# Optimization experiments

Measured on AMD Instinct MI355X. Metric: run time of the kernel, lower is better.

Reference implementation:

```python
import jax, jax.numpy as jnp
import numpy as np

N, K, IN_C, OUT_C = 100000, 128, 128, 128


def setup_inputs() -> dict:
    key = jax.random.key(0)
    k1, k2, k3 = jax.random.split(key, 3)
    x = jax.random.normal(k1, (N, IN_C), dtype=jnp.float32)
    U = jax.random.normal(k2, (N, K), dtype=jnp.float32)
    coeffs = jax.random.normal(k3, (OUT_C, K, IN_C), dtype=jnp.float32)
    return {"x": x, "U": U, "coeffs": coeffs}


def reference(x, U, coeffs):
    # U.T @ x : (K, in_channels)
    spec = jnp.einsum('nk,ni->ki', U, x)
    # coeffs * spec, summed over in_channels : (out_channels, K)
    mixed = jnp.einsum('oki,ki->ok', coeffs, spec)
    # U @ mixed : (out_channels, N)
    out = jnp.einsum('nk,ok->on', U, mixed)
    # softmax over N (dim=-1), then transpose -> (N, out_channels)
    return jax.nn.softmax(out, axis=-1).T
```

## Files before the change

kernel.cpp:

```cpp
#include <hip/hip_runtime.h>
#include <math.h>

#define N_PTS 100000
#define KDIM 128
#define CDIM 128
#define TILE_N 64
#define NB1 ((N_PTS + TILE_N - 1) / TILE_N)

typedef short s16x8 __attribute__((ext_vector_type(8)));
typedef float f32x4 __attribute__((ext_vector_type(4)));

static __device__ __forceinline__ unsigned short f2bf(float f) {
    unsigned int u = __float_as_uint(f);
    unsigned int r = (u + 0x7FFFu + ((u >> 16) & 1u)) >> 16;
    return (unsigned short)r;
}
static __device__ __forceinline__ float bf2f(unsigned short h) {
    return __uint_as_float(((unsigned int)h) << 16);
}

static __device__ __forceinline__ void split_trunc(float v, unsigned short& hi, unsigned short& lo) {
    unsigned int u = __float_as_uint(v);
    unsigned int uh = u & 0xFFFF0000u;
    float lf = v - __uint_as_float(uh);
    hi = (unsigned short)(u >> 16);
    lo = (unsigned short)(__float_as_uint(lf) >> 16);
}

static __device__ __forceinline__ void block_sync_lds() {
    asm volatile("s_waitcnt lgkmcnt(0)" ::: "memory");
    __builtin_amdgcn_s_barrier();
    asm volatile("" ::: "memory");
}

__global__ __launch_bounds__(512, 4) void kA(const float* __restrict__ U,
                                             const float* __restrict__ x,
                                             float* __restrict__ partials,
                                             int chunk) {
    __shared__ unsigned short SB[2][4][4096];
    const int tid = threadIdx.x;
    const int b = blockIdx.x;
    const int n_begin = b * chunk;
    const int n_end = min(N_PTS, n_begin + chunk);
    const int lane = tid & 63;
    const int w = tid >> 6;
    const int mtb = (w & 3) * 2;
    const int ntb = (w >> 2) * 4;
    const int quad = lane >> 4;
    const int nl = lane & 15;

    const int sc = tid & 127;
    const int rq = tid >> 7;
    const int sgran = (sc >> 4) * 64 + rq * 16 + (sc & 15);

    f32x4 acc[2][4];
#pragma unroll
    for (int mi = 0; mi < 2; ++mi)
#pragma unroll
        for (int ni = 0; ni < 4; ++ni) acc[mi][ni] = (f32x4)(0.0f);

    float uvA[8], xvA[8], uvB[8], xvB[8];

    auto loadChunk = [&](int ci, float* uv, float* xv) {
        const int r0 = n_begin + ci * 32 + rq * 8;
#pragma unroll
        for (int jj = 0; jj < 8; ++jj) {
            int gn = r0 + jj;
            bool ok = (gn < n_end);
            uv[jj] = ok ? U[(size_t)gn * 128 + sc] : 0.0f;
            xv[jj] = ok ? x[(size_t)gn * 128 + sc] : 0.0f;
        }
    };

    auto splitWrite = [&](int buf, const float* uv, const float* xv) {
        s16x8 uh, ul, xh, xl;
#pragma unroll
        for (int jj = 0; jj < 8; ++jj) {
            unsigned short h, l;
            split_trunc(uv[jj], h, l);
            uh[jj] = (short)h; ul[jj] = (short)l;
            split_trunc(xv[jj], h, l);
            xh[jj] = (short)h; xl[jj] = (short)l;
        }
        *(s16x8*)&SB[buf][0][sgran * 8] = uh;
        *(s16x8*)&SB[buf][1][sgran * 8] = ul;
        *(s16x8*)&SB[buf][2][sgran * 8] = xh;
        *(s16x8*)&SB[buf][3][sgran * 8] = xl;
    };

    auto compute = [&](int buf) {
        s16x8 ah[2], al[2];
#pragma unroll
        for (int mi = 0; mi < 2; ++mi) {
            const int off = ((mtb + mi) * 64 + lane) * 8;
            ah[mi] = *(s16x8*)&SB[buf][0][off];
            al[mi] = *(s16x8*)&SB[buf][1][off];
        }
#pragma unroll
        for (int ni = 0; ni < 4; ++ni) {
            const int off = ((ntb + ni) * 64 + lane) * 8;
            s16x8 bh = *(s16x8*)&SB[buf][2][off];
            s16x8 bl = *(s16x8*)&SB[buf][3][off];
#pragma unroll
            for (int mi = 0; mi < 2; ++mi) {
                acc[mi][ni] = __builtin_amdgcn_mfma_f32_16x16x32_bf16(ah[mi], bh, acc[mi][ni], 0, 0, 0);
                acc[mi][ni] = __builtin_amdgcn_mfma_f32_16x16x32_bf16(al[mi], bh, acc[mi][ni], 0, 0, 0);
                acc[mi][ni] = __builtin_amdgcn_mfma_f32_16x16x32_bf16(ah[mi], bl, acc[mi][ni], 0, 0, 0);
            }
        }
    };

    loadChunk(0, uvA, xvA);
    splitWrite(0, uvA, xvA);
    loadChunk(1, uvB, xvB);
    block_sync_lds();

    const int nTrips = chunk >> 6;
    for (int t = 0; t < nTrips; ++t) {
        loadChunk(2 * t + 2, uvA, xvA);
        compute(0);
        splitWrite(1, uvB, xvB);
        block_sync_lds();
        loadChunk(2 * t + 3, uvB, xvB);
        compute(1);
        if (t + 1 < nTrips) splitWrite(0, uvA, xvA);
        block_sync_lds();
    }

    float* p = partials + (size_t)b * 16384;
#pragma unroll
    for (int mi = 0; mi < 2; ++mi) {
#pragma unroll
        for (int reg = 0; reg < 4; ++reg) {
            int k = (mtb + mi) * 16 + quad * 4 + reg;
#pragma unroll
            for (int ni = 0; ni < 4; ++ni) {
                int i = (ntb + ni) * 16 + nl;
                p[k * 128 + i] = acc[mi][ni][reg];
            }
        }
    }
}

__global__ __launch_bounds__(256) void kA2a(const float* __restrict__ partials,
                                            float* __restrict__ partial2, int nA) {
    const int jc = blockIdx.x >> 3;
    const int s = blockIdx.x & 7;
    const int j = jc * 256 + threadIdx.x;
    const int per = (nA + 7) >> 3;
    int b = s * per;
    const int be = min(b + per, nA);
    float a0 = 0.0f, a1 = 0.0f, a2 = 0.0f, a3 = 0.0f;
    for (; b + 4 <= be; b += 4) {
        a0 += partials[(size_t)(b + 0) * 16384 + j];
        a1 += partials[(size_t)(b + 1) * 16384 + j];
        a2 += partials[(size_t)(b + 2) * 16384 + j];
        a3 += partials[(size_t)(b + 3) * 16384 + j];
    }
    for (; b < be; ++b) a0 += partials[(size_t)b * 16384 + j];
    partial2[(size_t)s * 16384 + j] = (a0 + a1) + (a2 + a3);
}

__global__ __launch_bounds__(256) void kB(const float* __restrict__ coeffs,
                                          const float* __restrict__ partial2,
                                          unsigned short* __restrict__ afrag_hi,
                                          unsigned short* __restrict__ afrag_lo) {
    int wave = (blockIdx.x * 256 + threadIdx.x) >> 6;
    int lane = threadIdx.x & 63;
    int o = wave >> 7;
    int k = wave & 127;
    const int j = k * 128 + lane * 2;
    float2 p0 = *(const float2*)&partial2[j];
    float2 p1 = *(const float2*)&partial2[16384 + j];
    float2 p2 = *(const float2*)&partial2[2 * 16384 + j];
    float2 p3 = *(const float2*)&partial2[3 * 16384 + j];
    float2 p4 = *(const float2*)&partial2[4 * 16384 + j];
    float2 p5 = *(const float2*)&partial2[5 * 16384 + j];
    float2 p6 = *(const float2*)&partial2[6 * 16384 + j];
    float2 p7 = *(const float2*)&partial2[7 * 16384 + j];
    float sx = ((p0.x + p1.x) + (p2.x + p3.x)) + ((p4.x + p5.x) + (p6.x + p7.x));
    float sy = ((p0.y + p1.y) + (p2.y + p3.y)) + ((p4.y + p5.y) + (p6.y + p7.y));
    float2 c2 = *(const float2*)&coeffs[((size_t)o * 128 + k) * 128 + lane * 2];
    float v = c2.x * sx + c2.y * sy;
#pragma unroll
    for (int s = 32; s >= 1; s >>= 1) v += __shfl_xor(v, s);
    if (lane == 0) {
        unsigned short hi = f2bf(v);
        unsigned short lo = f2bf(v - bf2f(hi));
        int idx = ((o >> 4) * 4 + (k >> 5)) * 512 + (((k >> 3) & 3) * 16 + (o & 15)) * 8 + (k & 7);
        afrag_hi[idx] = hi;
        afrag_lo[idx] = lo;
    }
}

__global__ __launch_bounds__(512) void kC1(const float* __restrict__ U,
                                           const unsigned short* __restrict__ afrag_hi,
                                           const unsigned short* __restrict__ afrag_lo,
                                           float* __restrict__ out,
                                           float* __restrict__ m_part,
                                           float* __restrict__ l_part) {
    __shared__ unsigned short Bh[8192];
    __shared__ unsigned short Bl[8192];
    const int tid = threadIdx.x;
    const int b = blockIdx.x;
    const int n0 = b * TILE_N;
    const int lane = tid & 63;
    const int w = tid >> 6;
    const int quad = lane >> 4;
    const int nl = lane & 15;

    {
        const int sn = tid & 63;
        const int k8b = tid >> 6;
        const int gn = n0 + sn;
#pragma unroll
        for (int r = 0; r < 2; ++r) {
            const int k0 = (k8b + r * 8) * 8;
            float4 f0 = make_float4(0, 0, 0, 0), f1 = make_float4(0, 0, 0, 0);
            if (gn < N_PTS) {
                f0 = *(const float4*)&U[(size_t)gn * 128 + k0];
                f1 = *(const float4*)&U[(size_t)gn * 128 + k0 + 4];
            }
            float vv[8] = {f0.x, f0.y, f0.z, f0.w, f1.x, f1.y, f1.z, f1.w};
            s16x8 hh, ll;
#pragma unroll
            for (int jj = 0; jj < 8; ++jj) {
                unsigned short h, l;
                split_trunc(vv[jj], h, l);
                hh[jj] = (short)h;
                ll[jj] = (short)l;
            }
            const int T = (k0 >> 5) * 4 + (sn >> 4);
            const int g = T * 64 + ((k0 >> 3) & 3) * 16 + ((sn & 15) ^ (T & 3));
            *(s16x8*)&Bh[g * 8] = hh;
            *(s16x8*)&Bl[g * 8] = ll;
        }
    }

    s16x8 Ah[4], Al[4];
#pragma unroll
    for (int kc = 0; kc < 4; ++kc) {
        size_t aoff = (size_t)(w * 4 + kc) * 512 + lane * 8;
        Ah[kc] = *(const s16x8*)(afrag_hi + aoff);
        Al[kc] = *(const s16x8*)(afrag_lo + aoff);
    }

    __syncthreads();

    f32x4 acc[4];
#pragma unroll
    for (int nt = 0; nt < 4; ++nt) acc[nt] = (f32x4)(0.0f);

#pragma unroll
    for (int kc = 0; kc < 4; ++kc) {
#pragma unroll
        for (int nt = 0; nt < 4; ++nt) {
            const int T = kc * 4 + nt;
            const int g = T * 64 + quad * 16 + (nl ^ (T & 3));
            s16x8 bh = *(s16x8*)&Bh[g * 8];
            s16x8 bl = *(s16x8*)&Bl[g * 8];
            acc[nt] = __builtin_amdgcn_mfma_f32_16x16x32_bf16(Ah[kc], bh, acc[nt], 0, 0, 0);
            acc[nt] = __builtin_amdgcn_mfma_f32_16x16x32_bf16(Al[kc], bh, acc[nt], 0, 0, 0);
            acc[nt] = __builtin_amdgcn_mfma_f32_16x16x32_bf16(Ah[kc], bl, acc[nt], 0, 0, 0);
        }
    }

#pragma unroll
    for (int nt = 0; nt < 4; ++nt) {
        if (n0 + nt * 16 + nl >= N_PTS) {
#pragma unroll
            for (int reg = 0; reg < 4; ++reg) acc[nt][reg] = -3.4e38f;
        }
    }

    float mb[4];
#pragma unroll
    for (int reg = 0; reg < 4; ++reg)
        mb[reg] = fmaxf(fmaxf(acc[0][reg], acc[1][reg]), fmaxf(acc[2][reg], acc[3][reg]));
#pragma unroll
    for (int s = 1; s < 16; s <<= 1) {
#pragma unroll
        for (int reg = 0; reg < 4; ++reg) mb[reg] = fmaxf(mb[reg], __shfl_xor(mb[reg], s));
    }

#pragma unroll
    for (int nt = 0; nt < 4; ++nt) {
#pragma unroll
        for (int reg = 0; reg < 4; ++reg) acc[nt][reg] = __expf(acc[nt][reg] - mb[reg]);
        int gn = n0 + nt * 16 + nl;
        if (gn < N_PTS)
            *(f32x4*)&out[(size_t)gn * 128 + w * 16 + quad * 4] = acc[nt];
    }

    float ls[4];
#pragma unroll
    for (int reg = 0; reg < 4; ++reg)
        ls[reg] = ((acc[0][reg] + acc[1][reg]) + (acc[2][reg] + acc[3][reg]));
#pragma unroll
    for (int s = 1; s < 16; s <<= 1) {
#pragma unroll
        for (int reg = 0; reg < 4; ++reg) ls[reg] += __shfl_xor(ls[reg], s);
    }

    if (nl == 0) {
#pragma unroll
        for (int reg = 0; reg < 4; ++reg) {
            int o = w * 16 + quad * 4 + reg;
            m_part[(size_t)o * NB1 + b] = mb[reg];
            l_part[(size_t)o * NB1 + b] = ls[reg];
        }
    }
}

__global__ __launch_bounds__(256) void kC2(const float* __restrict__ m_part,
                                           const float* __restrict__ l_part,
                                           float* __restrict__ scale) {
    const int o = blockIdx.x;
    const int tid = threadIdx.x;
    const float* __restrict__ mp = m_part + (size_t)o * NB1;
    const float* __restrict__ lp = l_part + (size_t)o * NB1;
    __shared__ float sm[256];
    float m = -3.4e38f;
    for (int b = tid; b < NB1; b += 256) m = fmaxf(m, mp[b]);
    sm[tid] = m;
    __syncthreads();
    for (int s = 128; s >= 1; s >>= 1) {
        if (tid < s) sm[tid] = fmaxf(sm[tid], sm[tid + s]);
        __syncthreads();
    }
    m = sm[0];
    __syncthreads();
    float l = 0.0f;
    for (int b = tid; b < NB1; b += 256)
        l += lp[b] * __expf(mp[b] - m);
    sm[tid] = l;
    __syncthreads();
    for (int s = 128; s >= 1; s >>= 1) {
        if (tid < s) sm[tid] += sm[tid + s];
        __syncthreads();
    }
    l = sm[0];
    float inv = 1.0f / l;
    for (int b = tid; b < NB1; b += 256)
        scale[(size_t)o * NB1 + b] = __expf(mp[b] - m) * inv;
}

__global__ __launch_bounds__(256) void kC3(float* __restrict__ out,
                                           const float* __restrict__ scale) {
    const int b = blockIdx.x;
    const int tid = threadIdx.x;
    __shared__ float sc[128];
    if (tid < 128) sc[tid] = scale[(size_t)tid * NB1 + b];
    __syncthreads();
    const int n0 = b * TILE_N;
#pragma unroll
    for (int r = 0; r < 8; ++r) {
        int idx = (r * 256 + tid) * 4;
        int n = idx >> 7;
        int o = idx & 127;
        int gn = n0 + n;
        if (gn < N_PTS) {
            float4 v = *(float4*)&out[(size_t)gn * 128 + o];
            v.x *= sc[o];
            v.y *= sc[o + 1];
            v.z *= sc[o + 2];
            v.w *= sc[o + 3];
            *(float4*)&out[(size_t)gn * 128 + o] = v;
        }
    }
}

extern "C" void kernel_launch(void* const* d_in, const int* in_sizes, int n_in,
                              void* d_out, int out_size, void* d_ws, size_t ws_size,
                              hipStream_t stream) {
    const float* x = (const float*)d_in[0];
    const float* U = (const float*)d_in[1];
    const float* coeffs = (const float*)d_in[2];
    float* out = (float*)d_out;

    float* f = (float*)d_ws;
    float* spec = f;
    unsigned short* afrag_hi = (unsigned short*)(f + 16384);
    unsigned short* afrag_lo = (unsigned short*)(f + 16384 + 8192);
    float* m_part = f + 16384 + 16384;
    float* l_part = m_part + (size_t)128 * NB1;
    float* scale = l_part + (size_t)128 * NB1;
    float* partial2 = scale + (size_t)128 * NB1;
    float* partialsA = partial2 + 8 * 16384;
    (void)spec;

    size_t fixed_bytes = ((size_t)(16384 * 2) + (size_t)NB1 * 128 * 3 + (size_t)8 * 16384) * 4;
    int nA = 1024;
    if (ws_size > fixed_bytes) {
        size_t avail = (ws_size - fixed_bytes) / 65536;
        if ((size_t)nA > avail) nA = (int)avail;
    } else {
        nA = 1;
    }
    if (nA < 1) nA = 1;
    int chunk = (((N_PTS + nA - 1) / nA) + 63) & ~63;
    int nB = (N_PTS + chunk - 1) / chunk;

    kA<<<nB, 512, 0, stream>>>(U, x, partialsA, chunk);
    kA2a<<<512, 256, 0, stream>>>(partialsA, partial2, nB);
    kB<<<4096, 256, 0, stream>>>(coeffs, partial2, afrag_hi, afrag_lo);
    kC1<<<NB1, 512, 0, stream>>>(U, afrag_hi, afrag_lo, out, m_part, l_part);
    kC2<<<128, 256, 0, stream>>>(m_part, l_part, scale);
    kC3<<<NB1, 256, 0, stream>>>(out, scale);
}
```

Measured before the change: 207.9 us.

## Recompute U@mixed tile in final pass instead of storing and rescaling output

The output stage now runs the small GEMM twice: a first pass that only produces per-tile max and exp-sum statistics, and a second pass that recomputes the tile and writes the fully normalized softmax directly. This removes the write-then-read-modify-write of the full 51 MB output that the separate scaling kernel needed, at the cost of reading U and doing the MFMA work twice. Separately, kA drops LDS double buffering in favour of a single buffer with an extra barrier per chunk and asks for 8 waves per SIMD occupancy, trading intra-block overlap for more resident blocks.

```diff
diff --git a/kernel.cpp b/kernel.cpp
--- a/kernel.cpp
+++ b/kernel.cpp
@@ -33,11 +33,11 @@
     asm volatile("" ::: "memory");
 }
 
-__global__ __launch_bounds__(512, 4) void kA(const float* __restrict__ U,
+__global__ __launch_bounds__(512, 8) void kA(const float* __restrict__ U,
                                              const float* __restrict__ x,
                                              float* __restrict__ partials,
                                              int chunk) {
-    __shared__ unsigned short SB[2][4][4096];
+    __shared__ unsigned short SB[4][4096];
     const int tid = threadIdx.x;
     const int b = blockIdx.x;
     const int n_begin = b * chunk;
@@ -72,7 +72,7 @@
         }
     };
 
-    auto splitWrite = [&](int buf, const float* uv, const float* xv) {
+    auto splitWrite = [&](const float* uv, const float* xv) {
         s16x8 uh, ul, xh, xl;
 #pragma unroll
         for (int jj = 0; jj < 8; ++jj) {
@@ -82,25 +82,25 @@
             split_trunc(xv[jj], h, l);
             xh[jj] = (short)h; xl[jj] = (short)l;
         }
-        *(s16x8*)&SB[buf][0][sgran * 8] = uh;
-        *(s16x8*)&SB[buf][1][sgran * 8] = ul;
-        *(s16x8*)&SB[buf][2][sgran * 8] = xh;
-        *(s16x8*)&SB[buf][3][sgran * 8] = xl;
+        *(s16x8*)&SB[0][sgran * 8] = uh;
+        *(s16x8*)&SB[1][sgran * 8] = ul;
+        *(s16x8*)&SB[2][sgran * 8] = xh;
+        *(s16x8*)&SB[3][sgran * 8] = xl;
     };
 
-    auto compute = [&](int buf) {
+    auto compute = [&]() {
         s16x8 ah[2], al[2];
 #pragma unroll
         for (int mi = 0; mi < 2; ++mi) {
             const int off = ((mtb + mi) * 64 + lane) * 8;
-            ah[mi] = *(s16x8*)&SB[buf][0][off];
-            al[mi] = *(s16x8*)&SB[buf][1][off];
+            ah[mi] = *(s16x8*)&SB[0][off];
+            al[mi] = *(s16x8*)&SB[1][off];
         }
 #pragma unroll
         for (int ni = 0; ni < 4; ++ni) {
             const int off = ((ntb + ni) * 64 + lane) * 8;
-            s16x8 bh = *(s16x8*)&SB[buf][2][off];
-            s16x8 bl = *(s16x8*)&SB[buf][3][off];
+            s16x8 bh = *(s16x8*)&SB[2][off];
+            s16x8 bl = *(s16x8*)&SB[3][off];
 #pragma unroll
             for (int mi = 0; mi < 2; ++mi) {
                 acc[mi][ni] = __builtin_amdgcn_mfma_f32_16x16x32_bf16(ah[mi], bh, acc[mi][ni], 0, 0, 0);
@@ -111,19 +111,18 @@
     };
 
     loadChunk(0, uvA, xvA);
-    splitWrite(0, uvA, xvA);
-    loadChunk(1, uvB, xvB);
-    block_sync_lds();
 
     const int nTrips = chunk >> 6;
     for (int t = 0; t < nTrips; ++t) {
+        loadChunk(2 * t + 1, uvB, xvB);
+        splitWrite(uvA, xvA);
+        block_sync_lds();
+        compute();
+        block_sync_lds();
         loadChunk(2 * t + 2, uvA, xvA);
-        compute(0);
-        splitWrite(1, uvB, xvB);
+        splitWrite(uvB, xvB);
         block_sync_lds();
-        loadChunk(2 * t + 3, uvB, xvB);
-        compute(1);
-        if (t + 1 < nTrips) splitWrite(0, uvA, xvA);
+        compute();
         block_sync_lds();
     }
 
@@ -193,16 +192,12 @@
     }
 }
 
-__global__ __launch_bounds__(512) void kC1(const float* __restrict__ U,
-                                           const unsigned short* __restrict__ afrag_hi,
-                                           const unsigned short* __restrict__ afrag_lo,
-                                           float* __restrict__ out,
-                                           float* __restrict__ m_part,
-                                           float* __restrict__ l_part) {
-    __shared__ unsigned short Bh[8192];
-    __shared__ unsigned short Bl[8192];
-    const int tid = threadIdx.x;
-    const int b = blockIdx.x;
+static __device__ __forceinline__ void c1_compute_tile(
+    const float* __restrict__ U,
+    const unsigned short* __restrict__ afrag_hi,
+    const unsigned short* __restrict__ afrag_lo,
+    unsigned short* Bh, unsigned short* Bl,
+    int b, int tid, f32x4 (&acc)[4]) {
     const int n0 = b * TILE_N;
     const int lane = tid & 63;
     const int w = tid >> 6;
@@ -247,7 +242,6 @@
 
     __syncthreads();
 
-    f32x4 acc[4];
 #pragma unroll
     for (int nt = 0; nt < 4; ++nt) acc[nt] = (f32x4)(0.0f);
 
@@ -264,6 +258,25 @@
             acc[nt] = __builtin_amdgcn_mfma_f32_16x16x32_bf16(Ah[kc], bl, acc[nt], 0, 0, 0);
         }
     }
+}
+
+__global__ __launch_bounds__(512) void kC1a(const float* __restrict__ U,
+                                            const unsigned short* __restrict__ afrag_hi,
+                                            const unsigned short* __restrict__ afrag_lo,
+                                            float* __restrict__ m_part,
+                                            float* __restrict__ l_part) {
+    __shared__ unsigned short Bh[8192];
+    __shared__ unsigned short Bl[8192];
+    const int tid = threadIdx.x;
+    const int b = blockIdx.x;
+    const int n0 = b * TILE_N;
+    const int lane = tid & 63;
+    const int w = tid >> 6;
+    const int quad = lane >> 4;
+    const int nl = lane & 15;
+
+    f32x4 acc[4];
+    c1_compute_tile(U, afrag_hi, afrag_lo, Bh, Bl, b, tid, acc);
 
 #pragma unroll
     for (int nt = 0; nt < 4; ++nt) {
@@ -283,19 +296,15 @@
         for (int reg = 0; reg < 4; ++reg) mb[reg] = fmaxf(mb[reg], __shfl_xor(mb[reg], s));
     }
 
-#pragma unroll
-    for (int nt = 0; nt < 4; ++nt) {
-#pragma unroll
-        for (int reg = 0; reg < 4; ++reg) acc[nt][reg] = __expf(acc[nt][reg] - mb[reg]);
-        int gn = n0 + nt * 16 + nl;
-        if (gn < N_PTS)
-            *(f32x4*)&out[(size_t)gn * 128 + w * 16 + quad * 4] = acc[nt];
-    }
-
     float ls[4];
 #pragma unroll
-    for (int reg = 0; reg < 4; ++reg)
-        ls[reg] = ((acc[0][reg] + acc[1][reg]) + (acc[2][reg] + acc[3][reg]));
+    for (int reg = 0; reg < 4; ++reg) {
+        float e0 = __expf(acc[0][reg] - mb[reg]);
+        float e1 = __expf(acc[1][reg] - mb[reg]);
+        float e2 = __expf(acc[2][reg] - mb[reg]);
+        float e3 = __expf(acc[3][reg] - mb[reg]);
+        ls[reg] = (e0 + e1) + (e2 + e3);
+    }
 #pragma unroll
     for (int s = 1; s < 16; s <<= 1) {
 #pragma unroll
@@ -345,28 +354,41 @@
         scale[(size_t)o * NB1 + b] = __expf(mp[b] - m) * inv;
 }
 
-__global__ __launch_bounds__(256) void kC3(float* __restrict__ out,
-                                           const float* __restrict__ scale) {
+__global__ __launch_bounds__(512) void kC1b(const float* __restrict__ U,
+                                            const unsigned short* __restrict__ afrag_hi,
+                                            const unsigned short* __restrict__ afrag_lo,
+                                            const float* __restrict__ m_part,
+                                            const float* __restrict__ scale,
+                                            float* __restrict__ out) {
+    __shared__ unsigned short Bh[8192];
+    __shared__ unsigned short Bl[8192];
+    const int tid = threadIdx.x;
     const int b = blockIdx.x;
-    const int tid = threadIdx.x;
-    __shared__ float sc[128];
-    if (tid < 128) sc[tid] = scale[(size_t)tid * NB1 + b];
-    __syncthreads();
     const int n0 = b * TILE_N;
-#pragma unroll
-    for (int r = 0; r < 8; ++r) {
-        int idx = (r * 256 + tid) * 4;
-        int n = idx >> 7;
-        int o = idx & 127;
-        int gn = n0 + n;
-        if (gn < N_PTS) {
-            float4 v = *(float4*)&out[(size_t)gn * 128 + o];
-            v.x *= sc[o];
-            v.y *= sc[o + 1];
-            v.z *= sc[o + 2];
-            v.w *= sc[o + 3];
-            *(float4*)&out[(size_t)gn * 128 + o] = v;
-        }
+    const int lane = tid & 63;
+    const int w = tid >> 6;
+    const int quad = lane >> 4;
+    const int nl = lane & 15;
+
+    f32x4 acc[4];
+    c1_compute_tile(U, afrag_hi, afrag_lo, Bh, Bl, b, tid, acc);
+
+    float mbv[4], scv[4];
+#pragma unroll
+    for (int reg = 0; reg < 4; ++reg) {
+        int o = w * 16 + quad * 4 + reg;
+        mbv[reg] = m_part[(size_t)o * NB1 + b];
+        scv[reg] = scale[(size_t)o * NB1 + b];
+    }
+
+#pragma unroll
+    for (int nt = 0; nt < 4; ++nt) {
+#pragma unroll
+        for (int reg = 0; reg < 4; ++reg)
+            acc[nt][reg] = __expf(acc[nt][reg] - mbv[reg]) * scv[reg];
+        int gn = n0 + nt * 16 + nl;
+        if (gn < N_PTS)
+            *(f32x4*)&out[(size_t)gn * 128 + w * 16 + quad * 4] = acc[nt];
     }
 }
 
@@ -404,7 +426,7 @@
     kA<<<nB, 512, 0, stream>>>(U, x, partialsA, chunk);
     kA2a<<<512, 256, 0, stream>>>(partialsA, partial2, nB);
     kB<<<4096, 256, 0, stream>>>(coeffs, partial2, afrag_hi, afrag_lo);
-    kC1<<<NB1, 512, 0, stream>>>(U, afrag_hi, afrag_lo, out, m_part, l_part);
+    kC1a<<<NB1, 512, 0, stream>>>(U, afrag_hi, afrag_lo, m_part, l_part);
     kC2<<<128, 256, 0, stream>>>(m_part, l_part, scale);
-    kC3<<<NB1, 256, 0, stream>>>(out, scale);
-}
+    kC1b<<<NB1, 512, 0, stream>>>(U, afrag_hi, afrag_lo, m_part, scale, out);
+}
```

Result: slower. 286.3 us (+37.7%).
